# Optimization experiments

Measured on AMD Instinct MI355X. Metric: run time of the kernel, lower is better.

Reference implementation:

```python
import jax, jax.numpy as jnp
import numpy as np

N_NODES = 50000
N_EDGES = 500000
F = 64          # in_feats == out_feats
H = 4           # num_heads
L = 4           # gnn_layer
NEG_SLOPE = 0.2 # DGL GATConv default leaky_relu slope


def setup_inputs() -> dict:
    key = jax.random.key(0)
    ks = jax.random.split(key, 7)
    feat = jax.random.normal(ks[0], (N_NODES, F), dtype=jnp.float32)
    W = jax.random.normal(ks[1], (L, F, H * F), dtype=jnp.float32) * (1.0 / np.sqrt(F))
    attn_l = jax.random.normal(ks[2], (L, H, F), dtype=jnp.float32) * 0.1
    attn_r = jax.random.normal(ks[3], (L, H, F), dtype=jnp.float32) * 0.1
    bias = jnp.zeros((L, H, F), dtype=jnp.float32)
    src = jax.random.randint(ks[4], (N_EDGES,), 0, N_NODES, dtype=jnp.int64)
    dst = jax.random.randint(ks[5], (N_EDGES,), 0, N_NODES, dtype=jnp.int64)
    return {"feat": feat, "W": W, "attn_l": attn_l, "attn_r": attn_r,
            "bias": bias, "src": src, "dst": dst}


def _gat_layer(h, src, dst, W_l, al, ar, b):
    # h: [N, F]; W_l: [F, H*F]; al/ar/b: [H, F]
    n = h.shape[0]
    ft = (h @ W_l).reshape(n, H, F)                       # [N, H, F]
    el = jnp.einsum("nhd,hd->nh", ft, al)                 # [N, H]
    er = jnp.einsum("nhd,hd->nh", ft, ar)                 # [N, H]
    e = jax.nn.leaky_relu(el[src] + er[dst], NEG_SLOPE)   # [E, H]
    # numerically-stable edge softmax over incoming edges of each dst
    emax = jax.ops.segment_max(e, dst, num_segments=n)    # [N, H], -inf if empty
    emax = jnp.where(jnp.isfinite(emax), emax, 0.0)
    ee = jnp.exp(e - emax[dst])                           # [E, H]
    denom = jax.ops.segment_sum(ee, dst, num_segments=n)  # [N, H]
    denom = jnp.where(denom > 0, denom, 1.0)
    alpha = ee / denom[dst]                               # [E, H]
    msg = ft[src] * alpha[:, :, None]                     # [E, H, F]
    rst = jax.ops.segment_sum(msg, dst, num_segments=n)   # [N, H, F]
    rst = rst + b                                         # GATConv output bias
    return jnp.sum(rst, axis=1)                           # sum over heads -> [N, F]


def reference(feat, W, attn_l, attn_r, bias, src, dst):
    h = feat
    for l in range(L):
        h = _gat_layer(h, src, dst, W[l], attn_l[l], attn_r[l], bias[l])
    return h
```

## Files before the change

kernel.cpp:

```cpp
#include <hip/hip_runtime.h>
#include <hip/hip_fp16.h>

#define NEG_SLOPE 0.2f

typedef _Float16 f16x8 __attribute__((ext_vector_type(8)));
typedef float f32x4 __attribute__((ext_vector_type(4)));


__global__ __launch_bounds__(256) void k_pro(
        const int* __restrict__ dst, int* __restrict__ deg,
        const float* __restrict__ W, const float* __restrict__ al,
        const float* __restrict__ ar, const float* __restrict__ bias,
        float* __restrict__ bsum, float* __restrict__ WABall, int ne) {
    int i = blockIdx.x * blockDim.x + threadIdx.x;
    if (i < ne) { atomicAdd(&deg[dst[i]], 1); return; }
    int j = i - ne;
    if (j < 256) {
        int l = j >> 6, f = j & 63;
        float s = 0.f;
        #pragma unroll
        for (int h = 0; h < 4; ++h) s += bias[(l << 8) + h * 64 + f];
        bsum[j] = s;
        return;
    }
    int j2 = j - 256;
    if (j2 < 2048) {
        int l = j2 >> 9, r = j2 & 511, k = r >> 3, jj = r & 7, hh = jj & 3;
        const float* wrow = W + (l << 14) + (k << 8) + hh * 64;
        const float* av = ((jj < 4) ? al : ar) + (l << 8) + hh * 64;
        float s = 0.f;
        #pragma unroll 8
        for (int f = 0; f < 64; ++f) s = fmaf(wrow[f], av[f], s);
        WABall[j2] = s;
    }
}

__global__ __launch_bounds__(256) void k_packT(
        const float* __restrict__ W, const float* __restrict__ WABall,
        const float* __restrict__ bsum,
        _Float16* __restrict__ Bf, _Float16* __restrict__ WABf0,
        float* __restrict__ cl) {
    int i = blockIdx.x * blockDim.x + threadIdx.x;
    if (i < 4 * 20480) {
        int l = i / 20480, r = i % 20480;
        int j = r & 7, lane = (r >> 3) & 63, kc = (r >> 9) & 7, ct = r >> 12;
        int k = kc * 32 + ((lane >> 4) << 3) + j;
        int c = ct * 16 + (lane & 15);
        int fi = k & 63, hh = k >> 6;
        float v = 0.f;
        if (c < 64) {
            v = W[(l << 14) + (fi << 8) + hh * 64 + c];
        } else if (c < 72 && l < 3) {
            int jj = c - 64;
            const float* wr = W + (l << 14) + (fi << 8) + hh * 64;
            const float* wa = WABall + (((l + 1) * 64) << 3) + jj;
            float s = 0.f;
            #pragma unroll 8
            for (int fo = 0; fo < 64; ++fo) s = fmaf(wr[fo], wa[fo << 3], s);
            v = s;
        }
        Bf[i] = (_Float16)v;
        return;
    }
    int i2 = i - 4 * 20480;
    if (i2 < 1024) {
        int j = i2 & 7, lane = (i2 >> 3) & 63, kc = i2 >> 9;
        int k = kc * 32 + ((lane >> 4) << 3) + j;
        int col = lane & 15;
        float v = (col < 8) ? WABall[(k << 3) + col] : 0.f;
        WABf0[i2] = (_Float16)v;
        return;
    }
    int i3 = i2 - 1024;
    if (i3 < 24) {
        int l = i3 >> 3, jj = i3 & 7;
        const float* wa = WABall + (((l + 1) * 64) << 3) + jj;
        float s = 0.f;
        #pragma unroll 8
        for (int fo = 0; fo < 64; ++fo) s = fmaf(bsum[l * 64 + fo], wa[fo << 3], s);
        cl[l * 8 + jj] = s;
    }
}

#define SCB 2048
__global__ __launch_bounds__(256) void k_scan1(const int* __restrict__ deg,
                                               int* __restrict__ bsums, int n) {
    __shared__ int wsum[4];
    int b = blockIdx.x, t = threadIdx.x;
    int i0 = b * SCB + t * 8;
    int s = 0;
    #pragma unroll
    for (int j = 0; j < 8; ++j) { int i = i0 + j; if (i < n) s += deg[i]; }
    #pragma unroll
    for (int m = 1; m < 64; m <<= 1) s += __shfl_xor(s, m);
    if ((t & 63) == 0) wsum[t >> 6] = s;
    __syncthreads();
    if (t == 0) bsums[b] = wsum[0] + wsum[1] + wsum[2] + wsum[3];
}

__global__ __launch_bounds__(256) void k_scan23(const int* __restrict__ deg,
                                                const int* __restrict__ bsums,
                                                int* __restrict__ rowptr,
                                                int* __restrict__ cursor,
                                                int n, int nb) {
    __shared__ int woff[4];
    __shared__ int boffs;
    int b = blockIdx.x, t = threadIdx.x, lane = t & 63, w = t >> 6;
    if (t < 64) {
        int v = (lane < nb) ? bsums[lane] : 0;
        int s = v;
        #pragma unroll
        for (int m = 1; m < 64; m <<= 1) {
            int y = __shfl_up(s, m);
            if (lane >= m) s += y;
        }
        if (lane == b) boffs = s - v;
        if (b == 0 && lane == nb - 1) rowptr[n] = s;
    }
    __syncthreads();
    int i0 = b * SCB + t * 8;
    int v[8]; int s8 = 0;
    #pragma unroll
    for (int j = 0; j < 8; ++j) { int i = i0 + j; v[j] = (i < n) ? deg[i] : 0; s8 += v[j]; }
    int s = s8;
    #pragma unroll
    for (int m = 1; m < 64; m <<= 1) { int y = __shfl_up(s, m); if (lane >= m) s += y; }
    if (lane == 63) woff[w] = s;
    __syncthreads();
    int wo = 0;
    #pragma unroll
    for (int k = 0; k < 4; ++k) if (k < w) wo += woff[k];
    int excl = boffs + wo + s - s8;
    #pragma unroll
    for (int j = 0; j < 8; ++j) {
        int i = i0 + j;
        if (i < n) { rowptr[i] = excl; cursor[i] = excl; }
        excl += v[j];
    }
}

__global__ __launch_bounds__(256) void k_scatter(const int* __restrict__ src,
                                                 const int* __restrict__ dst,
                                                 int* __restrict__ cursor,
                                                 int* __restrict__ csr_src, int ne) {
    int e = blockIdx.x * blockDim.x + threadIdx.x;
    if (e >= ne) return;
    int pos = atomicAdd(&cursor[dst[e]], 1);
    csr_src[pos] = src[e];
}


__global__ __launch_bounds__(256) void k0(
        const float* __restrict__ feat, const _Float16* __restrict__ WABf0,
        _Float16* __restrict__ x16, float* __restrict__ el, float* __restrict__ er,
        int n) {
    int t = threadIdx.x, w = t >> 6, lane = t & 63;
    int r0 = blockIdx.x * 64 + w * 16;
    if (r0 >= n) return;
    int m = lane & 15, kb = lane >> 4;
    int gr = r0 + m;

    f16x8 A0, A1;
    if (gr < n) {
        const float* hp = feat + (size_t)gr * 64 + kb * 8;
        float4 p0 = *(const float4*)(hp);
        float4 p1 = *(const float4*)(hp + 4);
        float4 q0 = *(const float4*)(hp + 32);
        float4 q1 = *(const float4*)(hp + 36);
        A0[0] = (_Float16)p0.x; A0[1] = (_Float16)p0.y;
        A0[2] = (_Float16)p0.z; A0[3] = (_Float16)p0.w;
        A0[4] = (_Float16)p1.x; A0[5] = (_Float16)p1.y;
        A0[6] = (_Float16)p1.z; A0[7] = (_Float16)p1.w;
        A1[0] = (_Float16)q0.x; A1[1] = (_Float16)q0.y;
        A1[2] = (_Float16)q0.z; A1[3] = (_Float16)q0.w;
        A1[4] = (_Float16)q1.x; A1[5] = (_Float16)q1.y;
        A1[6] = (_Float16)q1.z; A1[7] = (_Float16)q1.w;
    } else {
        #pragma unroll
        for (int j = 0; j < 8; ++j) { A0[j] = (_Float16)0.f; A1[j] = (_Float16)0.f; }
    }

    {
        f16x8 wb0 = *(const f16x8*)(WABf0 + lane * 8);
        f16x8 wb1 = *(const f16x8*)(WABf0 + 512 + lane * 8);
        f32x4 e; e[0] = 0.f; e[1] = 0.f; e[2] = 0.f; e[3] = 0.f;
        e = __builtin_amdgcn_mfma_f32_16x16x32_f16(A0, wb0, e, 0, 0, 0);
        e = __builtin_amdgcn_mfma_f32_16x16x32_f16(A1, wb1, e, 0, 0, 0);
        if (m < 8) {
            float* dp = (m < 4) ? el : er;
            #pragma unroll
            for (int r = 0; r < 4; ++r) {
                int g2 = r0 + kb * 4 + r;
                if (g2 < n) dp[(size_t)g2 * 4 + (m & 3)] = e[r];
            }
        }
    }

    if (gr < n) {
        *(f16x8*)(x16 + (size_t)gr * 64 + kb * 8) = A0;
        *(f16x8*)(x16 + (size_t)gr * 64 + 32 + kb * 8) = A1;
    }
}

__global__ __launch_bounds__(256) void k_agg2(
        const int* __restrict__ rowptr, const int* __restrict__ csr_src,
        const float* __restrict__ el, const float* __restrict__ er,
        const _Float16* __restrict__ x16, _Float16* __restrict__ agg, int n) {
    __shared__ float lds_ee[4][96];
    __shared__ int   lds_s[4][24];
    int wid  = (int)((blockIdx.x * blockDim.x + threadIdx.x) >> 6);
    int w    = (threadIdx.x >> 6) & 3;
    int lane = threadIdx.x & 63;
    if (wid >= n) return;
    int d = wid;
    int rbeg = rowptr[d], rend = rowptr[d + 1];
    if (rend == rbeg) {
        *(uint2*)(agg + (size_t)d * 256 + lane * 4) = make_uint2(0u, 0u);
        return;
    }

    int ei = lane >> 2, hh = lane & 3;
    int q = lane & 31, half = lane >> 5;
    float erh = er[(size_t)d * 4 + hh];

    int idx0 = rbeg + ei;
    bool v0 = idx0 < rend;
    int s0 = v0 ? csr_src[idx0] : 0;
    int sfb = __shfl(s0, 0);
    if (lane < 32) lds_ee[w][64 + lane] = 0.f;
    if (lane < 8)  lds_s[w][16 + lane] = sfb;

    float ee0 = 0.f;
    if (v0) {
        float x = el[(size_t)s0 * 4 + hh] + erh;
        x = x > 0.f ? x : NEG_SLOPE * x;
        ee0 = __expf(x);
    }
    float dsum = ee0;
    float2 acc[4];
    #pragma unroll
    for (int h = 0; h < 4; ++h) acc[h] = make_float2(0.f, 0.f);
    lds_ee[w][lane] = ee0;
    if (hh == 0) lds_s[w][ei] = v0 ? s0 : sfb;
    {
        int csz = min(16, rend - rbeg);
        int np = (csz + 1) >> 1;
        for (int p0 = 0; p0 < np; p0 += 2) {
            #pragma unroll
            for (int j = 0; j < 2; ++j) {
                int i = 2 * (p0 + j) + half;
                float4 ee4 = *(float4*)&lds_ee[w][i * 4];
                int s = lds_s[w][i];
                unsigned u = *(const unsigned*)(x16 + (size_t)s * 64 + q * 2);
                float2 xv = __half22float2(*(__half2*)&u);
                acc[0].x += ee4.x * xv.x; acc[0].y += ee4.x * xv.y;
                acc[1].x += ee4.y * xv.x; acc[1].y += ee4.y * xv.y;
                acc[2].x += ee4.z * xv.x; acc[2].y += ee4.z * xv.y;
                acc[3].x += ee4.w * xv.x; acc[3].y += ee4.w * xv.y;
            }
        }
    }
    for (int base = rbeg + 16; base < rend; base += 16) {
        int idx = base + ei;
        int e16 = min(16, rend - base);
        float ee = 0.f;
        if (idx < rend) {
            int s = csr_src[idx];
            float x = el[(size_t)s * 4 + hh] + erh;
            x = x > 0.f ? x : NEG_SLOPE * x;
            ee = __expf(x);
            if (hh == 0) lds_s[w][ei] = s;
        }
        dsum += ee;
        lds_ee[w][lane] = ee;
        int np = (e16 + 1) >> 1;
        for (int p0 = 0; p0 < np; p0 += 2) {
            #pragma unroll
            for (int j = 0; j < 2; ++j) {
                int i = 2 * (p0 + j) + half;
                float4 ee4 = *(float4*)&lds_ee[w][i * 4];
                int s = lds_s[w][i];
                unsigned u = *(const unsigned*)(x16 + (size_t)s * 64 + q * 2);
                float2 xv = __half22float2(*(__half2*)&u);
                acc[0].x += ee4.x * xv.x; acc[0].y += ee4.x * xv.y;
                acc[1].x += ee4.y * xv.x; acc[1].y += ee4.y * xv.y;
                acc[2].x += ee4.z * xv.x; acc[2].y += ee4.z * xv.y;
                acc[3].x += ee4.w * xv.x; acc[3].y += ee4.w * xv.y;
            }
        }
    }
    #pragma unroll
    for (int msk = 4; msk < 64; msk <<= 1) dsum += __shfl_xor(dsum, msk);
    float dh0 = __shfl(dsum, 0), dh1 = __shfl(dsum, 1);
    float dh2 = __shfl(dsum, 2), dh3 = __shfl(dsum, 3);
    #pragma unroll
    for (int h = 0; h < 4; ++h) {
        acc[h].x += __shfl_xor(acc[h].x, 32);
        acc[h].y += __shfl_xor(acc[h].y, 32);
    }
    if (half == 0) {
        float rd0 = 1.f / dh0, rd1 = 1.f / dh1, rd2 = 1.f / dh2, rd3 = 1.f / dh3;
        _Float16* ap = agg + (size_t)d * 256 + q * 2;
        __half2 v0h = __floats2half2_rn(acc[0].x * rd0, acc[0].y * rd0);
        __half2 v1h = __floats2half2_rn(acc[1].x * rd1, acc[1].y * rd1);
        __half2 v2h = __floats2half2_rn(acc[2].x * rd2, acc[2].y * rd2);
        __half2 v3h = __floats2half2_rn(acc[3].x * rd3, acc[3].y * rd3);
        *(__half2*)(ap)       = v0h;
        *(__half2*)(ap + 64)  = v1h;
        *(__half2*)(ap + 128) = v2h;
        *(__half2*)(ap + 192) = v3h;
    }
}

__global__ __launch_bounds__(256) void k_trans(
        const _Float16* __restrict__ agg, const _Float16* __restrict__ Bf,
        const float* __restrict__ bsum, const float* __restrict__ cl,
        _Float16* __restrict__ x16, float* __restrict__ el, float* __restrict__ er,
        float* __restrict__ outF, int n, int last) {
    int t = threadIdx.x, w = t >> 6, lane = t & 63;
    int r0 = blockIdx.x * 64 + w * 16;
    if (r0 >= n) return;
    int m = lane & 15, kb = lane >> 4;
    int gr = r0 + m;

    f16x8 A[8];
    if (gr < n) {
        const _Float16* ap = agg + (size_t)gr * 256 + kb * 8;
        #pragma unroll
        for (int kc = 0; kc < 8; ++kc) A[kc] = *(const f16x8*)(ap + kc * 32);
    } else {
        #pragma unroll
        for (int kc = 0; kc < 8; ++kc)
            #pragma unroll
            for (int j = 0; j < 8; ++j) A[kc][j] = (_Float16)0.f;
    }

    #pragma unroll
    for (int ct = 0; ct < 5; ++ct) {
        if (ct == 4 && last) break;
        f32x4 dd; dd[0] = 0.f; dd[1] = 0.f; dd[2] = 0.f; dd[3] = 0.f;
        #pragma unroll
        for (int kc = 0; kc < 8; ++kc) {
            f16x8 b = *(const f16x8*)(Bf + ((ct * 8 + kc) * 64 + lane) * 8);
            dd = __builtin_amdgcn_mfma_f32_16x16x32_f16(A[kc], b, dd, 0, 0, 0);
        }
        if (ct < 4) {
            int col = ct * 16 + m;
            float bv = bsum[col];
            #pragma unroll
            for (int r = 0; r < 4; ++r) {
                int g2 = r0 + kb * 4 + r;
                if (g2 < n) {
                    if (last) outF[(size_t)g2 * 64 + col] = dd[r] + bv;
                    else      x16[(size_t)g2 * 64 + col] = (_Float16)(dd[r] + bv);
                }
            }
        } else if (m < 8) {
            float cv = cl[m];
            float* dp = (m < 4) ? el : er;
            #pragma unroll
            for (int r = 0; r < 4; ++r) {
                int g2 = r0 + kb * 4 + r;
                if (g2 < n) dp[(size_t)g2 * 4 + (m & 3)] = dd[r] + cv;
            }
        }
    }
}


extern "C" void kernel_launch(void* const* d_in, const int* in_sizes, int n_in,
                              void* d_out, int out_size, void* d_ws, size_t ws_size,
                              hipStream_t stream) {
    const float* feat = (const float*)d_in[0];
    const float* W    = (const float*)d_in[1];
    const float* al   = (const float*)d_in[2];
    const float* ar   = (const float*)d_in[3];
    const float* bias = (const float*)d_in[4];
    const int*   src  = (const int*)d_in[5];
    const int*   dst  = (const int*)d_in[6];
    float* out = (float*)d_out;

    const int N = in_sizes[0] / 64;
    const int E = in_sizes[5];
    const int L = 4;

    float* ws = (float*)d_ws;
    _Float16* agg = (_Float16*)ws;
    _Float16* x16 = (_Float16*)(ws + (size_t)N * 128);
    float* el     = ws + (size_t)N * 160;
    float* er     = el + (size_t)N * 4;
    float* bsum   = er + (size_t)N * 4;
    float* WABall = bsum + 256;
    float* cl     = WABall + 2048;
    _Float16* Bf    = (_Float16*)(cl + 32);
    _Float16* WABf0 = (_Float16*)((float*)Bf + 40960);
    int* rowptr  = (int*)((float*)WABf0 + 512);
    int* cursor  = rowptr + (N + 1);
    int* deg     = cursor + N;
    int* csr_src = deg + N;
    int* bsums   = csr_src + E;

    const int NB = (N + SCB - 1) / SCB;

    hipMemsetAsync(deg, 0, (size_t)N * sizeof(int), stream);
    int pro_total = E + 256 + 2048;
    k_pro<<<(pro_total + 255) / 256, 256, 0, stream>>>(
        dst, deg, W, al, ar, bias, bsum, WABall, E);
    k_packT<<<(4 * 20480 + 1024 + 24 + 255) / 256, 256, 0, stream>>>(
        W, WABall, bsum, Bf, WABf0, cl);
    k_scan1<<<NB, 256, 0, stream>>>(deg, bsums, N);
    k_scan23<<<NB, 256, 0, stream>>>(deg, bsums, rowptr, cursor, N, NB);
    k_scatter<<<(E + 255) / 256, 256, 0, stream>>>(src, dst, cursor, csr_src, E);

    k0<<<(N + 63) / 64, 256, 0, stream>>>(feat, WABf0, x16, el, er, N);

    for (int l = 0; l < L; ++l) {
        int last = (l == L - 1);
        k_agg2<<<((size_t)N * 64 + 255) / 256, 256, 0, stream>>>(
            rowptr, csr_src, el, er, x16, agg, N);
        k_trans<<<(N + 63) / 64, 256, 0, stream>>>(
            agg, Bf + (size_t)l * 20480, bsum + (size_t)l * 64,
            cl + (size_t)(l < 3 ? l : 0) * 8,
            x16, el, er, out, N, last);
    }
}
```

Before: 246.3 us.

## Fuse edge aggregation and output transform into one per-layer kernel

Merges the aggregation kernel and the MFMA transform kernel into a single per-layer kernel. Each block aggregates 16 destination nodes into a shared-memory tile, then runs the matrix multiply from LDS, which removes the global round trip of the 256-wide fp16 agg buffer and one launch per layer. Inputs and outputs are ping-ponged between two buffers to avoid read/write races across blocks. In exchange, each wave now handles 4 nodes serially, which adds load imbalance, and the __syncthreads plus the extra LDS tile may lower occupancy.

```diff
diff --git a/kernel.cpp b/kernel.cpp
--- a/kernel.cpp
+++ b/kernel.cpp
@@ -202,162 +202,159 @@
     }
 }
 
-__global__ __launch_bounds__(256) void k_agg2(
+__global__ __launch_bounds__(256) void k_layer(
         const int* __restrict__ rowptr, const int* __restrict__ csr_src,
-        const float* __restrict__ el, const float* __restrict__ er,
-        const _Float16* __restrict__ x16, _Float16* __restrict__ agg, int n) {
+        const float* __restrict__ eli, const float* __restrict__ eri,
+        const _Float16* __restrict__ x16i, const _Float16* __restrict__ Bf,
+        const float* __restrict__ bsum, const float* __restrict__ cl,
+        _Float16* __restrict__ x16o, float* __restrict__ elo,
+        float* __restrict__ ero, float* __restrict__ outF, int n, int last) {
     __shared__ float lds_ee[4][96];
     __shared__ int   lds_s[4][24];
-    int wid  = (int)((blockIdx.x * blockDim.x + threadIdx.x) >> 6);
-    int w    = (threadIdx.x >> 6) & 3;
-    int lane = threadIdx.x & 63;
-    if (wid >= n) return;
-    int d = wid;
-    int rbeg = rowptr[d], rend = rowptr[d + 1];
-    if (rend == rbeg) {
-        *(uint2*)(agg + (size_t)d * 256 + lane * 4) = make_uint2(0u, 0u);
-        return;
-    }
-
+    __shared__ _Float16 at[16 * 272];
+    int t = threadIdx.x, w = t >> 6, lane = t & 63;
+    int r0 = blockIdx.x * 16;
     int ei = lane >> 2, hh = lane & 3;
     int q = lane & 31, half = lane >> 5;
-    float erh = er[(size_t)d * 4 + hh];
-
-    int idx0 = rbeg + ei;
-    bool v0 = idx0 < rend;
-    int s0 = v0 ? csr_src[idx0] : 0;
-    int sfb = __shfl(s0, 0);
+
     if (lane < 32) lds_ee[w][64 + lane] = 0.f;
-    if (lane < 8)  lds_s[w][16 + lane] = sfb;
-
-    float ee0 = 0.f;
-    if (v0) {
-        float x = el[(size_t)s0 * 4 + hh] + erh;
-        x = x > 0.f ? x : NEG_SLOPE * x;
-        ee0 = __expf(x);
-    }
-    float dsum = ee0;
-    float2 acc[4];
-    #pragma unroll
-    for (int h = 0; h < 4; ++h) acc[h] = make_float2(0.f, 0.f);
-    lds_ee[w][lane] = ee0;
-    if (hh == 0) lds_s[w][ei] = v0 ? s0 : sfb;
+
+    for (int j = 0; j < 4; ++j) {
+        int d = r0 + w * 4 + j;
+        _Float16* atr = at + (w * 4 + j) * 272;
+        int rbeg = 0, rend = 0;
+        if (d < n) { rbeg = rowptr[d]; rend = rowptr[d + 1]; }
+        if (rend == rbeg) {
+            if (half == 0) {
+                __half2 z = __floats2half2_rn(0.f, 0.f);
+                *(__half2*)(atr + q * 2)       = z;
+                *(__half2*)(atr + 64 + q * 2)  = z;
+                *(__half2*)(atr + 128 + q * 2) = z;
+                *(__half2*)(atr + 192 + q * 2) = z;
+            }
+            continue;
+        }
+        float erh = eri[(size_t)d * 4 + hh];
+
+        int idx0 = rbeg + ei;
+        bool v0 = idx0 < rend;
+        int s0 = v0 ? csr_src[idx0] : 0;
+        int sfb = __shfl(s0, 0);
+        if (lane < 8) lds_s[w][16 + lane] = sfb;
+
+        float ee0 = 0.f;
+        if (v0) {
+            float x = eli[(size_t)s0 * 4 + hh] + erh;
+            x = x > 0.f ? x : NEG_SLOPE * x;
+            ee0 = __expf(x);
+        }
+        float dsum = ee0;
+        float2 acc[4];
+        #pragma unroll
+        for (int h = 0; h < 4; ++h) acc[h] = make_float2(0.f, 0.f);
+        lds_ee[w][lane] = ee0;
+        if (hh == 0) lds_s[w][ei] = v0 ? s0 : sfb;
+        {
+            int csz = min(16, rend - rbeg);
+            int np = (csz + 1) >> 1;
+            for (int p0 = 0; p0 < np; p0 += 2) {
+                #pragma unroll
+                for (int jj = 0; jj < 2; ++jj) {
+                    int i = 2 * (p0 + jj) + half;
+                    float4 ee4 = *(float4*)&lds_ee[w][i * 4];
+                    int s = lds_s[w][i];
+                    unsigned u = *(const unsigned*)(x16i + (size_t)s * 64 + q * 2);
+                    float2 xv = __half22float2(*(__half2*)&u);
+                    acc[0].x += ee4.x * xv.x; acc[0].y += ee4.x * xv.y;
+                    acc[1].x += ee4.y * xv.x; acc[1].y += ee4.y * xv.y;
+                    acc[2].x += ee4.z * xv.x; acc[2].y += ee4.z * xv.y;
+                    acc[3].x += ee4.w * xv.x; acc[3].y += ee4.w * xv.y;
+                }
+            }
+        }
+        for (int base = rbeg + 16; base < rend; base += 16) {
+            int idx = base + ei;
+            int e16 = min(16, rend - base);
+            float ee = 0.f;
+            if (idx < rend) {
+                int s = csr_src[idx];
+                float x = eli[(size_t)s * 4 + hh] + erh;
+                x = x > 0.f ? x : NEG_SLOPE * x;
+                ee = __expf(x);
+                if (hh == 0) lds_s[w][ei] = s;
+            }
+            dsum += ee;
+            lds_ee[w][lane] = ee;
+            int np = (e16 + 1) >> 1;
+            for (int p0 = 0; p0 < np; p0 += 2) {
+                #pragma unroll
+                for (int jj = 0; jj < 2; ++jj) {
+                    int i = 2 * (p0 + jj) + half;
+                    float4 ee4 = *(float4*)&lds_ee[w][i * 4];
+                    int s = lds_s[w][i];
+                    unsigned u = *(const unsigned*)(x16i + (size_t)s * 64 + q * 2);
+                    float2 xv = __half22float2(*(__half2*)&u);
+                    acc[0].x += ee4.x * xv.x; acc[0].y += ee4.x * xv.y;
+                    acc[1].x += ee4.y * xv.x; acc[1].y += ee4.y * xv.y;
+                    acc[2].x += ee4.z * xv.x; acc[2].y += ee4.z * xv.y;
+                    acc[3].x += ee4.w * xv.x; acc[3].y += ee4.w * xv.y;
+                }
+            }
+        }
+        #pragma unroll
+        for (int msk = 4; msk < 64; msk <<= 1) dsum += __shfl_xor(dsum, msk);
+        float dh0 = __shfl(dsum, 0), dh1 = __shfl(dsum, 1);
+        float dh2 = __shfl(dsum, 2), dh3 = __shfl(dsum, 3);
+        #pragma unroll
+        for (int h = 0; h < 4; ++h) {
+            acc[h].x += __shfl_xor(acc[h].x, 32);
+            acc[h].y += __shfl_xor(acc[h].y, 32);
+        }
+        if (half == 0) {
+            float rd0 = 1.f / dh0, rd1 = 1.f / dh1, rd2 = 1.f / dh2, rd3 = 1.f / dh3;
+            *(__half2*)(atr + q * 2)       = __floats2half2_rn(acc[0].x * rd0, acc[0].y * rd0);
+            *(__half2*)(atr + 64 + q * 2)  = __floats2half2_rn(acc[1].x * rd1, acc[1].y * rd1);
+            *(__half2*)(atr + 128 + q * 2) = __floats2half2_rn(acc[2].x * rd2, acc[2].y * rd2);
+            *(__half2*)(atr + 192 + q * 2) = __floats2half2_rn(acc[3].x * rd3, acc[3].y * rd3);
+        }
+    }
+    __syncthreads();
+
+    int m = lane & 15, kb = lane >> 4;
+    f16x8 A[8];
+    #pragma unroll
+    for (int kc = 0; kc < 8; ++kc)
+        A[kc] = *(const f16x8*)&at[m * 272 + kc * 32 + kb * 8];
+
     {
-        int csz = min(16, rend - rbeg);
-        int np = (csz + 1) >> 1;
-        for (int p0 = 0; p0 < np; p0 += 2) {
-            #pragma unroll
-            for (int j = 0; j < 2; ++j) {
-                int i = 2 * (p0 + j) + half;
-                float4 ee4 = *(float4*)&lds_ee[w][i * 4];
-                int s = lds_s[w][i];
-                unsigned u = *(const unsigned*)(x16 + (size_t)s * 64 + q * 2);
-                float2 xv = __half22float2(*(__half2*)&u);
-                acc[0].x += ee4.x * xv.x; acc[0].y += ee4.x * xv.y;
-                acc[1].x += ee4.y * xv.x; acc[1].y += ee4.y * xv.y;
-                acc[2].x += ee4.z * xv.x; acc[2].y += ee4.z * xv.y;
-                acc[3].x += ee4.w * xv.x; acc[3].y += ee4.w * xv.y;
-            }
-        }
-    }
-    for (int base = rbeg + 16; base < rend; base += 16) {
-        int idx = base + ei;
-        int e16 = min(16, rend - base);
-        float ee = 0.f;
-        if (idx < rend) {
-            int s = csr_src[idx];
-            float x = el[(size_t)s * 4 + hh] + erh;
-            x = x > 0.f ? x : NEG_SLOPE * x;
-            ee = __expf(x);
-            if (hh == 0) lds_s[w][ei] = s;
-        }
-        dsum += ee;
-        lds_ee[w][lane] = ee;
-        int np = (e16 + 1) >> 1;
-        for (int p0 = 0; p0 < np; p0 += 2) {
-            #pragma unroll
-            for (int j = 0; j < 2; ++j) {
-                int i = 2 * (p0 + j) + half;
-                float4 ee4 = *(float4*)&lds_ee[w][i * 4];
-                int s = lds_s[w][i];
-                unsigned u = *(const unsigned*)(x16 + (size_t)s * 64 + q * 2);
-                float2 xv = __half22float2(*(__half2*)&u);
-                acc[0].x += ee4.x * xv.x; acc[0].y += ee4.x * xv.y;
-                acc[1].x += ee4.y * xv.x; acc[1].y += ee4.y * xv.y;
-                acc[2].x += ee4.z * xv.x; acc[2].y += ee4.z * xv.y;
-                acc[3].x += ee4.w * xv.x; acc[3].y += ee4.w * xv.y;
-            }
-        }
-    }
-    #pragma unroll
-    for (int msk = 4; msk < 64; msk <<= 1) dsum += __shfl_xor(dsum, msk);
-    float dh0 = __shfl(dsum, 0), dh1 = __shfl(dsum, 1);
-    float dh2 = __shfl(dsum, 2), dh3 = __shfl(dsum, 3);
-    #pragma unroll
-    for (int h = 0; h < 4; ++h) {
-        acc[h].x += __shfl_xor(acc[h].x, 32);
-        acc[h].y += __shfl_xor(acc[h].y, 32);
-    }
-    if (half == 0) {
-        float rd0 = 1.f / dh0, rd1 = 1.f / dh1, rd2 = 1.f / dh2, rd3 = 1.f / dh3;
-        _Float16* ap = agg + (size_t)d * 256 + q * 2;
-        __half2 v0h = __floats2half2_rn(acc[0].x * rd0, acc[0].y * rd0);
-        __half2 v1h = __floats2half2_rn(acc[1].x * rd1, acc[1].y * rd1);
-        __half2 v2h = __floats2half2_rn(acc[2].x * rd2, acc[2].y * rd2);
-        __half2 v3h = __floats2half2_rn(acc[3].x * rd3, acc[3].y * rd3);
-        *(__half2*)(ap)       = v0h;
-        *(__half2*)(ap + 64)  = v1h;
-        *(__half2*)(ap + 128) = v2h;
-        *(__half2*)(ap + 192) = v3h;
-    }
-}
-
-__global__ __launch_bounds__(256) void k_trans(
-        const _Float16* __restrict__ agg, const _Float16* __restrict__ Bf,
-        const float* __restrict__ bsum, const float* __restrict__ cl,
-        _Float16* __restrict__ x16, float* __restrict__ el, float* __restrict__ er,
-        float* __restrict__ outF, int n, int last) {
-    int t = threadIdx.x, w = t >> 6, lane = t & 63;
-    int r0 = blockIdx.x * 64 + w * 16;
-    if (r0 >= n) return;
-    int m = lane & 15, kb = lane >> 4;
-    int gr = r0 + m;
-
-    f16x8 A[8];
-    if (gr < n) {
-        const _Float16* ap = agg + (size_t)gr * 256 + kb * 8;
-        #pragma unroll
-        for (int kc = 0; kc < 8; ++kc) A[kc] = *(const f16x8*)(ap + kc * 32);
-    } else {
-        #pragma unroll
-        for (int kc = 0; kc < 8; ++kc)
-            #pragma unroll
-            for (int j = 0; j < 8; ++j) A[kc][j] = (_Float16)0.f;
-    }
-
-    #pragma unroll
-    for (int ct = 0; ct < 5; ++ct) {
-        if (ct == 4 && last) break;
+        int ct = w;
         f32x4 dd; dd[0] = 0.f; dd[1] = 0.f; dd[2] = 0.f; dd[3] = 0.f;
         #pragma unroll
         for (int kc = 0; kc < 8; ++kc) {
             f16x8 b = *(const f16x8*)(Bf + ((ct * 8 + kc) * 64 + lane) * 8);
             dd = __builtin_amdgcn_mfma_f32_16x16x32_f16(A[kc], b, dd, 0, 0, 0);
         }
-        if (ct < 4) {
-            int col = ct * 16 + m;
-            float bv = bsum[col];
-            #pragma unroll
-            for (int r = 0; r < 4; ++r) {
-                int g2 = r0 + kb * 4 + r;
-                if (g2 < n) {
-                    if (last) outF[(size_t)g2 * 64 + col] = dd[r] + bv;
-                    else      x16[(size_t)g2 * 64 + col] = (_Float16)(dd[r] + bv);
-                }
-            }
-        } else if (m < 8) {
+        int col = ct * 16 + m;
+        float bv = bsum[col];
+        #pragma unroll
+        for (int r = 0; r < 4; ++r) {
+            int g2 = r0 + kb * 4 + r;
+            if (g2 < n) {
+                if (last) outF[(size_t)g2 * 64 + col] = dd[r] + bv;
+                else      x16o[(size_t)g2 * 64 + col] = (_Float16)(dd[r] + bv);
+            }
+        }
+    }
+    if (w == 3 && !last) {
+        f32x4 dd; dd[0] = 0.f; dd[1] = 0.f; dd[2] = 0.f; dd[3] = 0.f;
+        #pragma unroll
+        for (int kc = 0; kc < 8; ++kc) {
+            f16x8 b = *(const f16x8*)(Bf + ((32 + kc) * 64 + lane) * 8);
+            dd = __builtin_amdgcn_mfma_f32_16x16x32_f16(A[kc], b, dd, 0, 0, 0);
+        }
+        if (m < 8) {
             float cv = cl[m];
-            float* dp = (m < 4) ? el : er;
+            float* dp = (m < 4) ? elo : ero;
             #pragma unroll
             for (int r = 0; r < 4; ++r) {
                 int g2 = r0 + kb * 4 + r;
@@ -385,11 +382,13 @@
     const int L = 4;
 
     float* ws = (float*)d_ws;
-    _Float16* agg = (_Float16*)ws;
-    _Float16* x16 = (_Float16*)(ws + (size_t)N * 128);
-    float* el     = ws + (size_t)N * 160;
-    float* er     = el + (size_t)N * 4;
-    float* bsum   = er + (size_t)N * 4;
+    _Float16* x16A = (_Float16*)ws;
+    _Float16* x16B = (_Float16*)(ws + (size_t)N * 32);
+    float* elA    = ws + (size_t)N * 64;
+    float* erA    = elA + (size_t)N * 4;
+    float* elB    = erA + (size_t)N * 4;
+    float* erB    = elB + (size_t)N * 4;
+    float* bsum   = erB + (size_t)N * 4;
     float* WABall = bsum + 256;
     float* cl     = WABall + 2048;
     _Float16* Bf    = (_Float16*)(cl + 32);
@@ -412,15 +411,19 @@
     k_scan23<<<NB, 256, 0, stream>>>(deg, bsums, rowptr, cursor, N, NB);
     k_scatter<<<(E + 255) / 256, 256, 0, stream>>>(src, dst, cursor, csr_src, E);
 
-    k0<<<(N + 63) / 64, 256, 0, stream>>>(feat, WABf0, x16, el, er, N);
-
+    k0<<<(N + 63) / 64, 256, 0, stream>>>(feat, WABf0, x16A, elA, erA, N);
+
+    _Float16* xin = x16A; float* eli = elA; float* eri = erA;
+    _Float16* xot = x16B; float* elo = elB; float* ero = erB;
     for (int l = 0; l < L; ++l) {
         int last = (l == L - 1);
-        k_agg2<<<((size_t)N * 64 + 255) / 256, 256, 0, stream>>>(
-            rowptr, csr_src, el, er, x16, agg, N);
-        k_trans<<<(N + 63) / 64, 256, 0, stream>>>(
-            agg, Bf + (size_t)l * 20480, bsum + (size_t)l * 64,
+        k_layer<<<(N + 15) / 16, 256, 0, stream>>>(
+            rowptr, csr_src, eli, eri, xin,
+            Bf + (size_t)l * 20480, bsum + (size_t)l * 64,
             cl + (size_t)(l < 3 ? l : 0) * 8,
-            x16, el, er, out, N, last);
-    }
-}
+            xot, elo, ero, out, N, last);
+        _Float16* tx = xin; xin = xot; xot = tx;
+        float* te = eli; eli = elo; elo = te;
+        te = eri; eri = ero; ero = te;
+    }
+}
```

Measured after the change: 232.3 us. -5.7%, faster.
